# Kernel optimization log

Measured on AMD Instinct MI355X. Metric: run time of the kernel, lower is better.

The kernel has to match this reference:

```python
import jax, jax.numpy as jnp
import numpy as np

GAMMA = 2
EPS = 1e-8


def setup_inputs() -> dict:
    key = jax.random.key(0)
    kx, kw = jax.random.split(key)
    B, C, D, W, H = 4, 256, 16, 16, 16
    x = jax.random.normal(kx, (B, C, D, W, H), dtype=jnp.float32)
    # Conv3d(chan, chan, kernel_size=1) == per-voxel linear: weight (C_out, C_in), bias (C_out,)
    Wt = jax.random.normal(kw, (C, C), dtype=jnp.float32) * 0.02
    b = jnp.zeros((C,), dtype=jnp.float32)
    return {"x": x, "W": Wt, "b": b}


def reference(x, W, b):
    B, C, D, Wd, H = x.shape
    N = D * Wd * H
    xf = x.reshape(B, C, N)                                  # b c n
    # torch cosine_similarity(dim=1): dot / max(|xi|*|xj|, eps)
    norm = jnp.linalg.norm(xf, axis=1, keepdims=True)        # b 1 n
    xn = xf / jnp.maximum(norm, EPS)
    sim = jnp.einsum('bcn,bcm->bnm', xn, xn)                 # b n n (cosine)
    sim = jax.nn.relu(sim) ** GAMMA
    # transform_net: 1x1x1 conv = channel-mixing GEMM per voxel
    t = jnp.einsum('oc,bcm->bom', W, xf) + b[None, :, None]  # b c m
    out = jnp.einsum('bnm,bcm->bcn', sim, t)                 # b c n
    return out.reshape(B, C, D, Wd, H)
```

## Files before the change

### kernel.cpp

```cpp
#include <hip/hip_runtime.h>
#include <hip/hip_bf16.h>


typedef unsigned short u16;
typedef __attribute__((ext_vector_type(8))) short short8;
typedef __attribute__((ext_vector_type(4))) float f32x4;

#define MFMA16(a, b, c) __builtin_amdgcn_mfma_f32_16x16x32_bf16((a), (b), (c), 0, 0, 0)

__device__ __forceinline__ u16 f2bf(float f) {
    union { float f; unsigned u; } v; v.f = f;
    unsigned u = v.u;
    u += 0x7fffu + ((u >> 16) & 1u);
    return (u16)(u >> 16);
}

__global__ __launch_bounds__(256) void k_prep(const float* __restrict__ x,
                                              const float* __restrict__ W,
                                              u16* __restrict__ xff,
                                              u16* __restrict__ Wf,
                                              float* __restrict__ nrm) {
    __shared__ float xs[256][65];
    __shared__ float part[4][64];
    __shared__ float rs_s[64];
    int bid = blockIdx.x;
    int b = bid >> 6, nt = bid & 63, n0 = nt << 6;
    int tid = threadIdx.x;

    if (bid < 32) {
        int q = (bid << 8) + tid;
        int lane = q & 63, kc = (q >> 6) & 7, ci = (q >> 9) & 3, wq = q >> 11;
        int row = (wq << 6) + (ci << 4) + (lane & 15);
        int col = (kc << 5) + ((lane >> 4) << 3);
        const float* wp = W + row * 256 + col;
        u16 tmp[8];
#pragma unroll
        for (int j = 0; j < 8; ++j) tmp[j] = f2bf(wp[j]);
        *(short8*)(Wf + ((size_t)q << 3)) = *(const short8*)tmp;
    }

    int rowg = tid >> 4, l16 = tid & 15;
    const float* xb = x + ((size_t)b << 20) + n0;
#pragma unroll
    for (int s = 0; s < 16; ++s) {
        int row = (s << 4) + rowg;
        float4 v = *(const float4*)(xb + (size_t)row * 4096 + (l16 << 2));
        xs[row][(l16 << 2) + 0] = v.x;
        xs[row][(l16 << 2) + 1] = v.y;
        xs[row][(l16 << 2) + 2] = v.z;
        xs[row][(l16 << 2) + 3] = v.w;
    }
    __syncthreads();
    int q2 = tid >> 6, nl = tid & 63;
    float ss = 0.f;
#pragma unroll 16
    for (int c = 0; c < 64; ++c) {
        float v = xs[(q2 << 6) + c][nl];
        ss += v * v;
    }
    part[q2][nl] = ss;
    __syncthreads();
    if (tid < 64) {
        float t = part[0][tid] + part[1][tid] + part[2][tid] + part[3][tid];
        float nr = sqrtf(t);
        nrm[(b << 12) + n0 + tid] = nr;
        rs_s[tid] = 1.0f / fmaxf(nr, 1e-8f);
    }
    __syncthreads();

    u16* xo = xff + ((size_t)b << 20) + ((size_t)nt << 14);
    int lane = tid & 63;
#pragma unroll
    for (int s = 0; s < 8; ++s) {
        int w2 = (s << 2) + (tid >> 6);
        int tl = ((w2 & 3) << 4) + (tid & 15);
        int c8 = ((w2 >> 2) << 2) + ((tid >> 4) & 3);
        float rsv = rs_s[tl];
        u16 tmp[8];
#pragma unroll
        for (int j = 0; j < 8; ++j)
            tmp[j] = f2bf(xs[(c8 << 3) + j][tl] * rsv);
        int chunk = ((tl >> 4) << 3) + (c8 >> 2);
        *(short8*)(xo + (chunk << 9) + (lane << 3)) = *(const short8*)tmp;
    }
}

__global__ __launch_bounds__(256) void k_tgemm(const u16* __restrict__ Wf,
                                               const u16* __restrict__ xff,
                                               const float* __restrict__ bias,
                                               const float* __restrict__ nrm,
                                               u16* __restrict__ tbf) {
    __shared__ u16 lds_t[256][72];
    int bid = blockIdx.x;
    int b = bid >> 6, mt = bid & 63;
    const u16* xf_t = xff + ((size_t)b << 20) + ((size_t)mt << 14);
    int tid = threadIdx.x, wid = tid >> 6, lane = tid & 63, lg = lane >> 4, lr = lane & 15;

    f32x4 zero = {0.f, 0.f, 0.f, 0.f};
    f32x4 acc[4][4];
#pragma unroll
    for (int ci = 0; ci < 4; ++ci)
#pragma unroll
        for (int mj = 0; mj < 4; ++mj) acc[ci][mj] = zero;

#pragma unroll
    for (int kc = 0; kc < 8; ++kc) {
        short8 afr[4], bfr[4];
#pragma unroll
        for (int ci = 0; ci < 4; ++ci)
            afr[ci] = *(const short8*)(Wf + ((size_t)((((wid << 2) + ci) << 3) + kc) << 9)
                                       + (lane << 3));
#pragma unroll
        for (int mj = 0; mj < 4; ++mj)
            bfr[mj] = *(const short8*)(xf_t + ((size_t)(((mj << 3) + kc)) << 9)
                                       + (lane << 3));
#pragma unroll
        for (int ci = 0; ci < 4; ++ci)
#pragma unroll
            for (int mj = 0; mj < 4; ++mj)
                acc[ci][mj] = MFMA16(afr[ci], bfr[mj], acc[ci][mj]);
    }
    float nv[4];
#pragma unroll
    for (int mj = 0; mj < 4; ++mj)
        nv[mj] = nrm[(b << 12) + (mt << 6) + (mj << 4) + lr];
#pragma unroll
    for (int ci = 0; ci < 4; ++ci) {
#pragma unroll
        for (int r = 0; r < 4; ++r) {
            int c = (wid << 6) + (ci << 4) + (lg << 2) + r;
            float bv = bias[c];
#pragma unroll
            for (int mj = 0; mj < 4; ++mj)
                lds_t[c][(mj << 4) + lr] = f2bf(acc[ci][mj][r] * nv[mj] + bv);
        }
    }
    __syncthreads();
    u16* to = tbf + ((size_t)b << 20) + ((size_t)mt << 14);
#pragma unroll
    for (int s = 0; s < 8; ++s) {
        int w2 = (s << 2) + (tid >> 6);
        int cq = w2 >> 3, ci2 = (w2 >> 1) & 3, k2 = w2 & 1;
        short8 v = *(const short8*)(&lds_t[(cq << 6) + (ci2 << 4) + lr][(k2 << 5) + (lg << 3)]);
        *(short8*)(to + (w2 << 9) + (lane << 3)) = v;
    }
}

__global__ __launch_bounds__(512) void k_fused(const u16* __restrict__ xff,
                                               const u16* __restrict__ tbf,
                                               float* __restrict__ out) {
    __shared__ __align__(16) u16 lds_p[2][4096];

#define PBYTE(row, col) ((((row) << 7) + ((col) << 1)) ^ (((row) & 7) << 4))
#define BAR() do { asm volatile("s_waitcnt lgkmcnt(0)" ::: "memory");              \
    __builtin_amdgcn_sched_barrier(0); __builtin_amdgcn_s_barrier();               \
    __builtin_amdgcn_sched_barrier(0); } while (0)

    int bid = blockIdx.x;
    int xcd = bid & 7, grp = bid >> 3;
    int batch = xcd >> 1;
    int nt = grp + 32 * (xcd & 1);
    int n0 = nt << 6;

    const u16* xf_b = xff + ((size_t)batch << 20);
    const u16* tb_f = tbf + ((size_t)batch << 20);
    float* out_b = out + ((size_t)batch << 20);

    int tid = threadIdx.x;
    int wid = tid >> 6, lane = tid & 63, lg = lane >> 4, lr = lane & 15;
    f32x4 zero = {0.f, 0.f, 0.f, 0.f};

    if (wid < 4) {
        int tc = wid;
        short8 afrag[4][8];
#pragma unroll
        for (int rt = 0; rt < 4; ++rt)
#pragma unroll
            for (int kc = 0; kc < 8; ++kc)
                afrag[rt][kc] = *(const short8*)(xf_b
                    + ((size_t)((((nt << 2) + rt) << 3) + kc) << 9) + (lane << 3));
        const u16* bstep = xf_b + ((size_t)(tc << 3) << 9) + (lane << 3);
        short8 bfrA[8], bfrB[8];
#pragma unroll
        for (int kc = 0; kc < 8; ++kc) bfrA[kc] = *(const short8*)(bstep + (kc << 9));
#pragma unroll
        for (int kc = 0; kc < 8; ++kc) bfrB[kc] = *(const short8*)(bstep + 16384 + (kc << 9));

#define SCOMP(BUF, PB)                                                                     \
    {                                                                                      \
        f32x4 sa0 = zero, sa1 = zero, sa2 = zero, sa3 = zero;                              \
        _Pragma("unroll")                                                                  \
        for (int kc = 0; kc < 8; ++kc) {                                                   \
            sa0 = MFMA16(afrag[0][kc], BUF[kc], sa0);                                      \
            sa1 = MFMA16(afrag[1][kc], BUF[kc], sa1);                                      \
            sa2 = MFMA16(afrag[2][kc], BUF[kc], sa2);                                      \
            sa3 = MFMA16(afrag[3][kc], BUF[kc], sa3);                                      \
        }                                                                                  \
        char* pd = (char*)&lds_p[PB][0];                                                   \
        int colw = (tc << 4) + lr;                                                         \
        _Pragma("unroll")                                                                  \
        for (int r = 0; r < 4; ++r) {                                                      \
            int rw = (lg << 2) + r;                                                        \
            float v0 = fmaxf(sa0[r], 0.f);                                                 \
            *(u16*)(pd + PBYTE(rw, colw)) = f2bf(v0 * v0);                                 \
            float v1 = fmaxf(sa1[r], 0.f);                                                 \
            *(u16*)(pd + PBYTE(rw + 16, colw)) = f2bf(v1 * v1);                            \
            float v2 = fmaxf(sa2[r], 0.f);                                                 \
            *(u16*)(pd + PBYTE(rw + 32, colw)) = f2bf(v2 * v2);                            \
            float v3 = fmaxf(sa3[r], 0.f);                                                 \
            *(u16*)(pd + PBYTE(rw + 48, colw)) = f2bf(v3 * v3);                            \
        }                                                                                  \
    }

        SCOMP(bfrA, 0);
        BAR();

#define SBODY(T, BC, BN)                                                                   \
    {                                                                                      \
        if ((T) <= 61) {                                                                   \
            _Pragma("unroll")                                                              \
            for (int kc = 0; kc < 8; ++kc)                                                 \
                BN[kc] = *(const short8*)(bstep + (size_t)((T) + 2) * 16384 + (kc << 9));  \
        }                                                                                  \
        if ((T) < 63) SCOMP(BC, ((T) + 1) & 1);                                            \
        BAR();                                                                             \
    }

        for (int t = 0; t < 64; t += 2) {
            SBODY(t, bfrB, bfrA);
            SBODY(t + 1, bfrA, bfrB);
        }
#undef SBODY
#undef SCOMP
    } else {
        int cq = wid - 4;
        const u16* tstep = tb_f + ((size_t)(cq << 3) << 9) + (lane << 3);
        short8 tbcA[4][2], tbcB[4][2];
#pragma unroll
        for (int ci = 0; ci < 4; ++ci)
#pragma unroll
            for (int k2 = 0; k2 < 2; ++k2)
                tbcA[ci][k2] = *(const short8*)(tstep + (((ci << 1) + k2) << 9));

        f32x4 oacc[4][4];
#pragma unroll
        for (int ci = 0; ci < 4; ++ci)
#pragma unroll
            for (int nj = 0; nj < 4; ++nj) oacc[ci][nj] = zero;
        BAR();

#define OBODY(T, TC, TN)                                                                   \
    {                                                                                      \
        if ((T) <= 62) {                                                                   \
            _Pragma("unroll")                                                              \
            for (int ci = 0; ci < 4; ++ci) {                                               \
                _Pragma("unroll")                                                          \
                for (int k2 = 0; k2 < 2; ++k2)                                             \
                    TN[ci][k2] = *(const short8*)(tstep + (size_t)((T) + 1) * 16384        \
                                                  + (((ci << 1) + k2) << 9));             \
            }                                                                              \
        }                                                                                  \
        char* pc = (char*)&lds_p[(T) & 1][0];                                              \
        short8 pfr[4][2];                                                                  \
        _Pragma("unroll")                                                                  \
        for (int nj = 0; nj < 4; ++nj) {                                                   \
            _Pragma("unroll")                                                              \
            for (int k2 = 0; k2 < 2; ++k2)                                                 \
                pfr[nj][k2] = *(const short8*)(pc + PBYTE((nj << 4) + lr,                  \
                                                          (k2 << 5) + (lg << 3)));        \
        }                                                                                  \
        _Pragma("unroll")                                                                  \
        for (int ci = 0; ci < 4; ++ci) {                                                   \
            _Pragma("unroll")                                                              \
            for (int nj = 0; nj < 4; ++nj) {                                               \
                oacc[ci][nj] = MFMA16(TC[ci][0], pfr[nj][0], oacc[ci][nj]);                \
                oacc[ci][nj] = MFMA16(TC[ci][1], pfr[nj][1], oacc[ci][nj]);                \
            }                                                                              \
        }                                                                                  \
        BAR();                                                                             \
    }

        for (int t = 0; t < 64; t += 2) {
            OBODY(t, tbcA, tbcB);
            OBODY(t + 1, tbcB, tbcA);
        }
#undef OBODY

#pragma unroll
        for (int ci = 0; ci < 4; ++ci) {
            int c = (cq << 6) + (ci << 4) + (lg << 2);
#pragma unroll
            for (int nj = 0; nj < 4; ++nj) {
                int n = n0 + (nj << 4) + lr;
                float* op = out_b + (size_t)c * 4096 + n;
#pragma unroll
                for (int r = 0; r < 4; ++r) op[(size_t)r * 4096] = oacc[ci][nj][r];
            }
        }
    }
#undef PBYTE
#undef BAR
}

extern "C" void kernel_launch(void* const* d_in, const int* in_sizes, int n_in,
                              void* d_out, int out_size, void* d_ws, size_t ws_size,
                              hipStream_t stream) {
    const float* x = (const float*)d_in[0];
    const float* W = (const float*)d_in[1];
    const float* bias = (const float*)d_in[2];
    float* out = (float*)d_out;

    char* ws = (char*)d_ws;
    u16* xff = (u16*)ws;
    u16* tbf = (u16*)(ws + ((size_t)8 << 20));
    u16* Wf = (u16*)(ws + ((size_t)16 << 20));
    float* nrm = (float*)(ws + ((size_t)16 << 20) + (192u << 10));

    hipLaunchKernelGGL(k_prep, dim3(256), dim3(256), 0, stream, x, W, xff, Wf, nrm);
    hipLaunchKernelGGL(k_tgemm, dim3(256), dim3(256), 0, stream, Wf, xff, bias, nrm, tbf);
    hipLaunchKernelGGL(k_fused, dim3(256), dim3(512), 0, stream, xff, tbf, out);
}
```

Baseline: 85.75 us.

## Process two S tiles per barrier with four-slot LDS ring and MFMA priority

```diff
diff --git a/kernel.cpp b/kernel.cpp
--- a/kernel.cpp
+++ b/kernel.cpp
@@ -149,7 +149,7 @@
 __global__ __launch_bounds__(512) void k_fused(const u16* __restrict__ xff,
                                                const u16* __restrict__ tbf,
                                                float* __restrict__ out) {
-    __shared__ __align__(16) u16 lds_p[2][4096];
+    __shared__ __align__(16) u16 lds_p[4][4096];
 
 #define PBYTE(row, col) ((((row) << 7) + ((col) << 1)) ^ (((row) & 7) << 4))
 #define BAR() do { asm volatile("s_waitcnt lgkmcnt(0)" ::: "memory");              \
@@ -186,9 +186,10 @@
 #pragma unroll
         for (int kc = 0; kc < 8; ++kc) bfrB[kc] = *(const short8*)(bstep + 16384 + (kc << 9));
 
-#define SCOMP(BUF, PB)                                                                     \
+#define SCOMP(BUF, SLOT)                                                                   \
     {                                                                                      \
         f32x4 sa0 = zero, sa1 = zero, sa2 = zero, sa3 = zero;                              \
+        __builtin_amdgcn_s_setprio(1);                                                     \
         _Pragma("unroll")                                                                  \
         for (int kc = 0; kc < 8; ++kc) {                                                   \
             sa0 = MFMA16(afrag[0][kc], BUF[kc], sa0);                                      \
@@ -196,7 +197,8 @@
             sa2 = MFMA16(afrag[2][kc], BUF[kc], sa2);                                      \
             sa3 = MFMA16(afrag[3][kc], BUF[kc], sa3);                                      \
         }                                                                                  \
-        char* pd = (char*)&lds_p[PB][0];                                                   \
+        __builtin_amdgcn_s_setprio(0);                                                     \
+        char* pd = (char*)&lds_p[0][0] + ((SLOT) << 13);                                   \
         int colw = (tc << 4) + lr;                                                         \
         _Pragma("unroll")                                                                  \
         for (int r = 0; r < 4; ++r) {                                                      \
@@ -213,24 +215,30 @@
     }
 
         SCOMP(bfrA, 0);
+#pragma unroll
+        for (int kc = 0; kc < 8; ++kc)
+            bfrA[kc] = *(const short8*)(bstep + 2 * 16384 + (kc << 9));
+        SCOMP(bfrB, 1);
+#pragma unroll
+        for (int kc = 0; kc < 8; ++kc)
+            bfrB[kc] = *(const short8*)(bstep + 3 * 16384 + (kc << 9));
         BAR();
 
-#define SBODY(T, BC, BN)                                                                   \
-    {                                                                                      \
-        if ((T) <= 61) {                                                                   \
-            _Pragma("unroll")                                                              \
-            for (int kc = 0; kc < 8; ++kc)                                                 \
-                BN[kc] = *(const short8*)(bstep + (size_t)((T) + 2) * 16384 + (kc << 9));  \
-        }                                                                                  \
-        if ((T) < 63) SCOMP(BC, ((T) + 1) & 1);                                            \
-        BAR();                                                                             \
-    }
-
-        for (int t = 0; t < 64; t += 2) {
-            SBODY(t, bfrB, bfrA);
-            SBODY(t + 1, bfrA, bfrB);
+        for (int pt = 2; pt <= 64; pt += 2) {
+            if (pt <= 63) SCOMP(bfrA, (pt & 3));
+            if (pt + 2 <= 63) {
+#pragma unroll
+                for (int kc = 0; kc < 8; ++kc)
+                    bfrA[kc] = *(const short8*)(bstep + (size_t)(pt + 2) * 16384 + (kc << 9));
+            }
+            if (pt + 1 <= 63) SCOMP(bfrB, ((pt + 1) & 3));
+            if (pt + 3 <= 63) {
+#pragma unroll
+                for (int kc = 0; kc < 8; ++kc)
+                    bfrB[kc] = *(const short8*)(bstep + (size_t)(pt + 3) * 16384 + (kc << 9));
+            }
+            BAR();
         }
-#undef SBODY
 #undef SCOMP
     } else {
         int cq = wid - 4;
@@ -239,8 +247,10 @@
 #pragma unroll
         for (int ci = 0; ci < 4; ++ci)
 #pragma unroll
-            for (int k2 = 0; k2 < 2; ++k2)
+            for (int k2 = 0; k2 < 2; ++k2) {
                 tbcA[ci][k2] = *(const short8*)(tstep + (((ci << 1) + k2) << 9));
+                tbcB[ci][k2] = *(const short8*)(tstep + 16384 + (((ci << 1) + k2) << 9));
+            }
 
         f32x4 oacc[4][4];
 #pragma unroll
@@ -249,18 +259,9 @@
             for (int nj = 0; nj < 4; ++nj) oacc[ci][nj] = zero;
         BAR();
 
-#define OBODY(T, TC, TN)                                                                   \
+#define OEAT(TC, SLOT)                                                                     \
     {                                                                                      \
-        if ((T) <= 62) {                                                                   \
-            _Pragma("unroll")                                                              \
-            for (int ci = 0; ci < 4; ++ci) {                                               \
-                _Pragma("unroll")                                                          \
-                for (int k2 = 0; k2 < 2; ++k2)                                             \
-                    TN[ci][k2] = *(const short8*)(tstep + (size_t)((T) + 1) * 16384        \
-                                                  + (((ci << 1) + k2) << 9));             \
-            }                                                                              \
-        }                                                                                  \
-        char* pc = (char*)&lds_p[(T) & 1][0];                                              \
+        char* pc = (char*)&lds_p[0][0] + ((SLOT) << 13);                                   \
         short8 pfr[4][2];                                                                  \
         _Pragma("unroll")                                                                  \
         for (int nj = 0; nj < 4; ++nj) {                                                   \
@@ -269,6 +270,7 @@
                 pfr[nj][k2] = *(const short8*)(pc + PBYTE((nj << 4) + lr,                  \
                                                           (k2 << 5) + (lg << 3)));        \
         }                                                                                  \
+        __builtin_amdgcn_s_setprio(1);                                                     \
         _Pragma("unroll")                                                                  \
         for (int ci = 0; ci < 4; ++ci) {                                                   \
             _Pragma("unroll")                                                              \
@@ -277,14 +279,31 @@
                 oacc[ci][nj] = MFMA16(TC[ci][1], pfr[nj][1], oacc[ci][nj]);                \
             }                                                                              \
         }                                                                                  \
-        BAR();                                                                             \
-    }
-
-        for (int t = 0; t < 64; t += 2) {
-            OBODY(t, tbcA, tbcB);
-            OBODY(t + 1, tbcB, tbcA);
+        __builtin_amdgcn_s_setprio(0);                                                     \
+    }
+
+        for (int ct = 0; ct <= 62; ct += 2) {
+            OEAT(tbcA, (ct & 3));
+            if (ct + 2 <= 63) {
+#pragma unroll
+                for (int ci = 0; ci < 4; ++ci)
+#pragma unroll
+                    for (int k2 = 0; k2 < 2; ++k2)
+                        tbcA[ci][k2] = *(const short8*)(tstep + (size_t)(ct + 2) * 16384
+                                                        + (((ci << 1) + k2) << 9));
+            }
+            OEAT(tbcB, ((ct + 1) & 3));
+            if (ct + 3 <= 63) {
+#pragma unroll
+                for (int ci = 0; ci < 4; ++ci)
+#pragma unroll
+                    for (int k2 = 0; k2 < 2; ++k2)
+                        tbcB[ci][k2] = *(const short8*)(tstep + (size_t)(ct + 3) * 16384
+                                                        + (((ci << 1) + k2) << 9));
+            }
+            BAR();
         }
-#undef OBODY
+#undef OEAT
 
 #pragma unroll
         for (int ci = 0; ci < 4; ++ci) {
```

Result: no change. 84.13 us (-1.9%).
